# Kernel tuning notes

Measured on AMD Instinct MI355X. Metric: run time of the kernel, lower is better.

The kernel has to match this reference:

```python
import jax, jax.numpy as jnp
import numpy as np

KERNEL_MUL = 2.0
KERNEL_NUM = 5
N, D = 4096, 512  # total batch (half source, half target), feature dim


def setup_inputs() -> dict:
    key = jax.random.key(0)
    latent = jax.random.normal(key, (N, D), dtype=jnp.float32)
    # first half domain 0 (source), second half domain 1 (target)
    domain = jnp.concatenate([jnp.zeros(N // 2, jnp.int64 if jax.config.jax_enable_x64 else jnp.int32),
                              jnp.ones(N // 2, jnp.int64 if jax.config.jax_enable_x64 else jnp.int32)])
    return {"latent": latent, "domain": domain}


def _gaussian_kernel_mean(a, b, kernel_mul, kernel_num):
    # Matches torch guassian_kernel followed by torch.mean(...)
    total = jnp.concatenate([a, b], axis=0)            # [m, d]
    m = total.shape[0]
    sq = jnp.sum(total * total, axis=1)                # [m]
    # ||x_i - x_j||^2 via GEMM trick (same math as expand-based version)
    d2 = sq[:, None] + sq[None, :] - 2.0 * (total @ total.T)  # [m, m]
    # torch uses L2_distance.data -> bandwidth is detached from autodiff
    bw = jnp.sum(jax.lax.stop_gradient(d2)) / (m * m - m)
    bw = bw / (kernel_mul ** (kernel_num // 2))
    k = jnp.zeros_like(d2)
    for i in range(kernel_num):
        k = k + jnp.exp(-d2 / (bw * (kernel_mul ** i)))
    return jnp.mean(k)


def reference(latent, domain):
    # domain is sorted: first half source (0), second half target (1)
    half = latent.shape[0] // 2
    src, tgt = latent[:half], latent[half:]
    xx = _gaussian_kernel_mean(src, src, KERNEL_MUL, KERNEL_NUM)
    yy = _gaussian_kernel_mean(tgt, tgt, KERNEL_MUL, KERNEL_NUM)
    xy = _gaussian_kernel_mean(src, tgt, KERNEL_MUL, KERNEL_NUM)
    return xx + yy - 2.0 * xy
```

## Files before the change

kernel.cpp:

```cpp
#include <hip/hip_runtime.h>
#include <hip/hip_bf16.h>
#include <cmath>

#define N_TOTAL 4096
#define HALF_N  2048
#define D_DIM   512


__global__ __launch_bounds__(256) void k_rowstats(const float* __restrict__ x,
                                                  float* __restrict__ sq,
                                                  float* __restrict__ colsum,
                                                  double* __restrict__ sumsq) {
    __shared__ float cs[512];
    const int tid = threadIdx.x;
    cs[tid] = 0.f; cs[tid + 256] = 0.f;
    __syncthreads();

    const int w = tid >> 6, l = tid & 63;
    const int rb = blockIdx.x * 16;

    float colacc[8] = {0.f,0.f,0.f,0.f,0.f,0.f,0.f,0.f};
    double mysq = 0.0;

    #pragma unroll
    for (int r4 = 0; r4 < 4; ++r4) {
        const int row = rb + w + 4 * r4;
        const float4* p = (const float4*)(x + (size_t)row * D_DIM);
        float4 v0 = p[2 * l];
        float4 v1 = p[2 * l + 1];
        colacc[0] += v0.x; colacc[1] += v0.y; colacc[2] += v0.z; colacc[3] += v0.w;
        colacc[4] += v1.x; colacc[5] += v1.y; colacc[6] += v1.z; colacc[7] += v1.w;
        float s = v0.x*v0.x + v0.y*v0.y + v0.z*v0.z + v0.w*v0.w
                + v1.x*v1.x + v1.y*v1.y + v1.z*v1.z + v1.w*v1.w;
        #pragma unroll
        for (int off = 32; off; off >>= 1) s += __shfl_xor(s, off);
        if (l == 0) { sq[row] = s; mysq += (double)s; }
    }

    const int half = (rb < HALF_N) ? 0 : 1;
    if (l == 0) atomicAdd(&sumsq[half], mysq);

    #pragma unroll
    for (int k2 = 0; k2 < 8; ++k2) atomicAdd(&cs[8 * l + k2], colacc[k2]);
    __syncthreads();

    float* dst = colsum + half * 512;
    atomicAdd(&dst[tid],       cs[tid]);
    atomicAdd(&dst[tid + 256], cs[tid + 256]);
}

__global__ __launch_bounds__(256) void k_bw(const float* __restrict__ colsum,
                                            const double* __restrict__ sumsq,
                                            float* __restrict__ bw) {
    const int tid = threadIdx.x;
    double pss = 0, ptt = 0, pst = 0;
    for (int c = tid; c < 512; c += 256) {
        double a = colsum[c], b = colsum[512 + c];
        pss += a * a; ptt += b * b; pst += a * b;
    }
    #pragma unroll
    for (int off = 32; off; off >>= 1) {
        pss += __shfl_xor(pss, off);
        ptt += __shfl_xor(ptt, off);
        pst += __shfl_xor(pst, off);
    }
    __shared__ double red[4][3];
    const int w = tid >> 6, l = tid & 63;
    if (l == 0) { red[w][0] = pss; red[w][1] = ptt; red[w][2] = pst; }
    __syncthreads();
    if (tid == 0) {
        double ss = red[0][0] + red[1][0] + red[2][0] + red[3][0];
        double tt = red[0][1] + red[1][1] + red[2][1] + red[3][1];
        double st = red[0][2] + red[1][2] + red[2][2] + red[3][2];
        const double n = (double)HALF_N;
        double Sss = 2.0 * n * sumsq[0] - 2.0 * ss;
        double Stt = 2.0 * n * sumsq[1] - 2.0 * tt;
        double Sst = n * (sumsq[0] + sumsq[1]) - 2.0 * st;
        const double denom = (double)N_TOTAL * (double)N_TOTAL - (double)N_TOTAL;
        bw[0] = (float)(Sss / denom);
        bw[1] = (float)(Stt / denom);
        bw[2] = (float)((Sss + Stt + 2.0 * Sst) / denom * 0.25);
    }
}

#define BM 128
#define BK 32
#define LDT 132
#define NTILE 32
#define NWORK 528

__global__ __launch_bounds__(256) void k_main(const float* __restrict__ x,
                                              const float* __restrict__ sq,
                                              const float* __restrict__ bw,
                                              double* __restrict__ acc) {
    const int t = blockIdx.x;
    int bi = (int)((65.0f - sqrtf((float)(4225 - 8 * t))) * 0.5f);
    if (bi < 0) bi = 0;
    if (bi > NTILE - 1) bi = NTILE - 1;
    while (bi > 0 && (32 * bi - bi * (bi - 1) / 2) > t) --bi;
    while (bi < NTILE - 1 && (32 * (bi + 1) - (bi + 1) * bi / 2) <= t) ++bi;
    const int bj = bi + (t - (32 * bi - bi * (bi - 1) / 2));

    __shared__ float As[BK][LDT];
    __shared__ float Bs[BK][LDT];

    const int tid = threadIdx.x;
    const int tx = tid & 15, ty = tid >> 4;
    const int i0 = bi * BM, j0 = bj * BM;

    float c[8][8];
    #pragma unroll
    for (int i = 0; i < 8; ++i)
        #pragma unroll
        for (int j = 0; j < 8; ++j) c[i][j] = 0.f;

    for (int k0 = 0; k0 < D_DIM; k0 += BK) {
        #pragma unroll
        for (int u = 0; u < 4; ++u) {
            const int f = tid + 256 * u;
            const int row = f >> 3;
            const int q = f & 7;
            float4 va = *(const float4*)(x + (size_t)(i0 + row) * D_DIM + k0 + 4 * q);
            float4 vb = *(const float4*)(x + (size_t)(j0 + row) * D_DIM + k0 + 4 * q);
            As[4*q+0][row] = va.x; As[4*q+1][row] = va.y; As[4*q+2][row] = va.z; As[4*q+3][row] = va.w;
            Bs[4*q+0][row] = vb.x; Bs[4*q+1][row] = vb.y; Bs[4*q+2][row] = vb.z; Bs[4*q+3][row] = vb.w;
        }
        __syncthreads();

        #pragma unroll 4
        for (int kk = 0; kk < BK; ++kk) {
            float4 a0 = *(const float4*)&As[kk][4 * ty];
            float4 a1 = *(const float4*)&As[kk][4 * ty + 64];
            float4 b0 = *(const float4*)&Bs[kk][4 * tx];
            float4 b1 = *(const float4*)&Bs[kk][4 * tx + 64];
            const float a[8] = {a0.x,a0.y,a0.z,a0.w,a1.x,a1.y,a1.z,a1.w};
            const float b[8] = {b0.x,b0.y,b0.z,b0.w,b1.x,b1.y,b1.z,b1.w};
            #pragma unroll
            for (int i = 0; i < 8; ++i)
                #pragma unroll
                for (int j = 0; j < 8; ++j)
                    c[i][j] = fmaf(a[i], b[j], c[i][j]);
        }
        __syncthreads();
    }

    const bool iS = (i0 < HALF_N), jS = (j0 < HALF_N);
    const bool diagRegion = (iS == jS);
    const double wgt = (bi == bj) ? 1.0 : 2.0;
    const float L2E = 1.4426950408889634f;
    const float cxy = -L2E / bw[2];
    const float cdg = diagRegion ? (-L2E / (iS ? bw[0] : bw[1])) : 0.f;

    float sqi[8], sqj[8];
    #pragma unroll
    for (int a = 0; a < 4; ++a) {
        sqi[a]     = sq[i0 + 4 * ty + a];
        sqi[a + 4] = sq[i0 + 64 + 4 * ty + a];
        sqj[a]     = sq[j0 + 4 * tx + a];
        sqj[a + 4] = sq[j0 + 64 + 4 * tx + a];
    }

    float sxy = 0.f, sdg = 0.f;
    #pragma unroll
    for (int i = 0; i < 8; ++i) {
        #pragma unroll
        for (int j = 0; j < 8; ++j) {
            const float d2 = sqi[i] + sqj[j] - 2.f * c[i][j];
            {
                const float tt = d2 * cxy;
                sxy += exp2f(tt) + exp2f(tt * 0.5f) + exp2f(tt * 0.25f)
                     + exp2f(tt * 0.125f) + exp2f(tt * 0.0625f);
            }
            if (diagRegion) {
                const float tt = d2 * cdg;
                sdg += exp2f(tt) + exp2f(tt * 0.5f) + exp2f(tt * 0.25f)
                     + exp2f(tt * 0.125f) + exp2f(tt * 0.0625f);
            }
        }
    }

    #pragma unroll
    for (int off = 32; off; off >>= 1) {
        sxy += __shfl_xor(sxy, off);
        sdg += __shfl_xor(sdg, off);
    }
    __shared__ float redA[4], redB[4];
    if ((tid & 63) == 0) { redA[tid >> 6] = sxy; redB[tid >> 6] = sdg; }
    __syncthreads();
    if (tid == 0) {
        double txy = (double)redA[0] + redA[1] + redA[2] + redA[3];
        atomicAdd(&acc[2], wgt * txy);
        if (diagRegion) {
            double tdg = (double)redB[0] + redB[1] + redB[2] + redB[3];
            atomicAdd(&acc[iS ? 0 : 1], wgt * tdg);
        }
    }
}

__global__ void k_final(const double* __restrict__ acc, float* __restrict__ out) {
    const double hh = (double)HALF_N * (double)HALF_N;
    const double ff = (double)N_TOTAL * (double)N_TOTAL;
    double xx = acc[0] / hh;
    double yy = acc[1] / hh;
    double xy = acc[2] / ff;
    out[0] = (float)(xx + yy - 2.0 * xy);
}

extern "C" void kernel_launch(void* const* d_in, const int* in_sizes, int n_in,
                              void* d_out, int out_size, void* d_ws, size_t ws_size,
                              hipStream_t stream) {
    const float* latent = (const float*)d_in[0];

    char* wsb = (char*)d_ws;
    float*  sq     = (float*)wsb;
    float*  colsum = (float*)(wsb + 16384);
    double* sumsq  = (double*)(wsb + 20480);
    double* acc    = (double*)(wsb + 20496);
    float*  bw     = (float*)(wsb + 20520);

    (void)hipMemsetAsync(wsb + 16384, 0, 20532 - 16384, stream);

    k_rowstats<<<256, 256, 0, stream>>>(latent, sq, colsum, sumsq);
    k_bw<<<1, 256, 0, stream>>>(colsum, sumsq, bw);
    k_main<<<NWORK, 256, 0, stream>>>(latent, sq, bw, acc);
    k_final<<<1, 1, 0, stream>>>(acc, (float*)d_out);
}
```

Measured before the change: 242.7 us.

## Prefetch next K-tile into registers and double-buffer LDS fragment loads

```diff
diff --git a/kernel.cpp b/kernel.cpp
--- a/kernel.cpp
+++ b/kernel.cpp
@@ -89,10 +89,10 @@
 #define NTILE 32
 #define NWORK 528
 
-__global__ __launch_bounds__(256) void k_main(const float* __restrict__ x,
-                                              const float* __restrict__ sq,
-                                              const float* __restrict__ bw,
-                                              double* __restrict__ acc) {
+__global__ __launch_bounds__(256, 2) void k_main(const float* __restrict__ x,
+                                                 const float* __restrict__ sq,
+                                                 const float* __restrict__ bw,
+                                                 double* __restrict__ acc) {
     const int t = blockIdx.x;
     int bi = (int)((65.0f - sqrtf((float)(4225 - 8 * t))) * 0.5f);
     if (bi < 0) bi = 0;
@@ -114,32 +114,62 @@
         #pragma unroll
         for (int j = 0; j < 8; ++j) c[i][j] = 0.f;
 
+    float4 rA[4], rB[4];
+    #pragma unroll
+    for (int u = 0; u < 4; ++u) {
+        const int f = tid + 256 * u;
+        const int row = f >> 3, q = f & 7;
+        rA[u] = *(const float4*)(x + (size_t)(i0 + row) * D_DIM + 4 * q);
+        rB[u] = *(const float4*)(x + (size_t)(j0 + row) * D_DIM + 4 * q);
+    }
+
     for (int k0 = 0; k0 < D_DIM; k0 += BK) {
         #pragma unroll
         for (int u = 0; u < 4; ++u) {
             const int f = tid + 256 * u;
-            const int row = f >> 3;
-            const int q = f & 7;
-            float4 va = *(const float4*)(x + (size_t)(i0 + row) * D_DIM + k0 + 4 * q);
-            float4 vb = *(const float4*)(x + (size_t)(j0 + row) * D_DIM + k0 + 4 * q);
-            As[4*q+0][row] = va.x; As[4*q+1][row] = va.y; As[4*q+2][row] = va.z; As[4*q+3][row] = va.w;
-            Bs[4*q+0][row] = vb.x; Bs[4*q+1][row] = vb.y; Bs[4*q+2][row] = vb.z; Bs[4*q+3][row] = vb.w;
+            const int row = f >> 3, q = f & 7;
+            As[4*q+0][row] = rA[u].x; As[4*q+1][row] = rA[u].y;
+            As[4*q+2][row] = rA[u].z; As[4*q+3][row] = rA[u].w;
+            Bs[4*q+0][row] = rB[u].x; Bs[4*q+1][row] = rB[u].y;
+            Bs[4*q+2][row] = rB[u].z; Bs[4*q+3][row] = rB[u].w;
         }
         __syncthreads();
+
+        if (k0 + BK < D_DIM) {
+            #pragma unroll
+            for (int u = 0; u < 4; ++u) {
+                const int f = tid + 256 * u;
+                const int row = f >> 3, q = f & 7;
+                rA[u] = *(const float4*)(x + (size_t)(i0 + row) * D_DIM + (k0 + BK) + 4 * q);
+                rB[u] = *(const float4*)(x + (size_t)(j0 + row) * D_DIM + (k0 + BK) + 4 * q);
+            }
+        }
+
+        float4 a0 = *(const float4*)&As[0][4 * ty];
+        float4 a1 = *(const float4*)&As[0][4 * ty + 64];
+        float4 b0 = *(const float4*)&Bs[0][4 * tx];
+        float4 b1 = *(const float4*)&Bs[0][4 * tx + 64];
 
         #pragma unroll 4
         for (int kk = 0; kk < BK; ++kk) {
-            float4 a0 = *(const float4*)&As[kk][4 * ty];
-            float4 a1 = *(const float4*)&As[kk][4 * ty + 64];
-            float4 b0 = *(const float4*)&Bs[kk][4 * tx];
-            float4 b1 = *(const float4*)&Bs[kk][4 * tx + 64];
-            const float a[8] = {a0.x,a0.y,a0.z,a0.w,a1.x,a1.y,a1.z,a1.w};
-            const float b[8] = {b0.x,b0.y,b0.z,b0.w,b1.x,b1.y,b1.z,b1.w};
+            float4 na0, na1, nb0, nb1;
+            if (kk < BK - 1) {
+                na0 = *(const float4*)&As[kk + 1][4 * ty];
+                na1 = *(const float4*)&As[kk + 1][4 * ty + 64];
+                nb0 = *(const float4*)&Bs[kk + 1][4 * tx];
+                nb1 = *(const float4*)&Bs[kk + 1][4 * tx + 64];
+            }
+            float a[8], b[8];
+            a[0]=a0.x; a[1]=a0.y; a[2]=a0.z; a[3]=a0.w;
+            a[4]=a1.x; a[5]=a1.y; a[6]=a1.z; a[7]=a1.w;
+            b[0]=b0.x; b[1]=b0.y; b[2]=b0.z; b[3]=b0.w;
+            b[4]=b1.x; b[5]=b1.y; b[6]=b1.z; b[7]=b1.w;
             #pragma unroll
             for (int i = 0; i < 8; ++i)
                 #pragma unroll
                 for (int j = 0; j < 8; ++j)
                     c[i][j] = fmaf(a[i], b[j], c[i][j]);
+            if (kk < BK - 1) { a0 = na0; a1 = na1; b0 = nb0; b1 = nb1; }
         }
         __syncthreads();
     }
```

Result: slower. 271.8 us (+12.0%).
